# Performance work log

Measured on AMD Instinct MI355X. Metric: run time of the kernel, lower is better.

Reference implementation:

```python
import jax, jax.numpy as jnp
import numpy as np

N = 50000      # nodes (single node type 'tx')
E = 400000     # edges per edge type ('fwd' and 'rev')
F_IN = 128     # input feature dim
F = 128        # cfg.gnn.dim_inner
H = 8          # attention heads
D = F // H     # per-head dim
L = 2          # cfg.gnn.layers_mp
C = 2          # dim_out (fraud logits)


def setup_inputs() -> dict:
    key = jax.random.key(0)
    k = jax.random.split(key, 12)
    f32 = jnp.float32
    g = lambda kk, sh, fan: jax.random.normal(kk, sh, f32) / np.float32(np.sqrt(fan))
    return dict(
        x=jax.random.normal(k[0], (N, F_IN), f32),
        edge_index_fwd=jax.random.randint(k[1], (2, E), 0, N),
        edge_index_rev=jax.random.randint(k[2], (2, E), 0, N),
        in_w=g(k[3], (F_IN, F), F_IN),
        in_b=jnp.zeros((F,), f32),
        kqv_w=g(k[4], (L, F, 3 * F), F),
        kqv_b=jnp.zeros((L, 3 * F), f32),
        krel_w=g(k[5], (L, 2, H, D, D), D),
        vrel_w=g(k[6], (L, 2, H, D, D), D),
        p_rel=jnp.ones((L, 2, H), f32),
        out_w=g(k[7], (L, F, F), F),
        out_b=jnp.zeros((L, F), f32),
        skip=jnp.ones((L,), f32),
        head_w=g(k[8], (F, C), F),
        head_b=jnp.zeros((C,), f32),
    )


def reference(x, edge_index_fwd, edge_index_rev, in_w, in_b, kqv_w, kqv_b,
              krel_w, vrel_w, p_rel, out_w, out_b, skip, head_w, head_b):
    n = x.shape[0]
    ef, er = edge_index_fwd, edge_index_rev
    Ef, Er = ef.shape[1], er.shape[1]
    dst = jnp.concatenate([ef[1], er[1]])                 # [E_tot]
    scale = 1.0 / jnp.sqrt(jnp.asarray(D, x.dtype))

    h = x @ in_w + in_b                                   # in_proj['tx'], [N,F]
    for l in range(L):
        kqv = h @ kqv_w[l] + kqv_b[l]                     # [N,3F]
        k, q, v = jnp.split(kqv, 3, axis=1)
        k = k.reshape(n, H, D)
        q = q.reshape(n, H, D)
        v = v.reshape(n, H, D)
        # per-edge-type relation transforms (head-wise DxD, no bias)
        k_rel = jnp.einsum('nhd,ehdf->enhf', k, krel_w[l])  # [2,N,H,D]
        v_rel = jnp.einsum('nhd,ehdf->enhf', v, vrel_w[l])
        # gather src features per edge type, concatenate edge types
        k_j = jnp.concatenate([k_rel[0][ef[0]], k_rel[1][er[0]]], axis=0)  # [E_tot,H,D]
        v_j = jnp.concatenate([v_rel[0][ef[0]], v_rel[1][er[0]]], axis=0)
        p_e = jnp.concatenate([jnp.broadcast_to(p_rel[l, 0], (Ef, H)),
                               jnp.broadcast_to(p_rel[l, 1], (Er, H))], axis=0)
        q_i = q[dst]                                       # [E_tot,H,D]
        alpha = jnp.einsum('ehd,ehd->eh', q_i, k_j) * p_e * scale
        # segment softmax over all incoming edges of each dst node
        m = jax.ops.segment_max(alpha, dst, num_segments=n)
        ex = jnp.exp(alpha - m[dst])
        denom = jax.ops.segment_sum(ex, dst, num_segments=n)
        w = ex / (denom[dst] + 1e-16)                      # [E_tot,H]
        agg = jax.ops.segment_sum(w[:, :, None] * v_j, dst,
                                  num_segments=n).reshape(n, F)
        a = jax.nn.gelu(agg, approximate=False) @ out_w[l] + out_b[l]
        g = jax.nn.sigmoid(skip[l])
        h = jax.nn.relu(g * a + (1.0 - g) * h)             # skip + act(dropout=0)
    return h @ head_w + head_b                             # logits [N,C]
```

## Files before the change

### kernel.cpp

```cpp
#include <hip/hip_runtime.h>
#include <math.h>

typedef short short8 __attribute__((ext_vector_type(8)));
typedef float f32x4 __attribute__((ext_vector_type(4)));

__device__ __forceinline__ unsigned short f2bf(float f){
    unsigned u = __float_as_uint(f);
    unsigned r = u + 0x7fffu + ((u >> 16) & 1u);
    return (unsigned short)(r >> 16);
}

__global__ void k_zero_i(int* __restrict__ p, int n)
{
    for (int i = blockIdx.x*blockDim.x + threadIdx.x; i < n; i += gridDim.x*blockDim.x)
        p[i] = 0;
}

__global__ void k_count(const int* __restrict__ ef, const int* __restrict__ er,
                        int* __restrict__ deg, int Ef, int Er)
{
    int Etot = Ef + Er;
    for (int e = blockIdx.x*blockDim.x + threadIdx.x; e < Etot; e += gridDim.x*blockDim.x) {
        int dst = (e < Ef) ? ef[Ef + e] : er[Er + (e - Ef)];
        atomicAdd(&deg[dst], 1);
    }
}

__global__ void k_chunk_sums(const int* __restrict__ deg, int* __restrict__ csum, int n)
{
    __shared__ int s[256];
    int t = threadIdx.x, i = blockIdx.x*256 + t;
    s[t] = (i < n) ? deg[i] : 0;
    __syncthreads();
    for (int off = 128; off > 0; off >>= 1) {
        if (t < off) s[t] += s[t + off];
        __syncthreads();
    }
    if (t == 0) csum[blockIdx.x] = s[0];
}

__global__ void k_scan_chunks(int* __restrict__ csum, int nch)
{
    __shared__ int s[1024];
    int t = threadIdx.x;
    int v = (t < nch) ? csum[t] : 0;
    s[t] = v; __syncthreads();
    for (int off = 1; off < 1024; off <<= 1) {
        int u = (t >= off) ? s[t - off] : 0;
        __syncthreads();
        s[t] += u;
        __syncthreads();
    }
    if (t < nch) csum[t] = s[t] - v;
}

__global__ void k_rowstart(const int* __restrict__ deg, const int* __restrict__ csum,
                           int* __restrict__ row_start, int* __restrict__ cursor, int n)
{
    __shared__ int s[256];
    int t = threadIdx.x, i = blockIdx.x*256 + t;
    int d = (i < n) ? deg[i] : 0;
    s[t] = d; __syncthreads();
    for (int off = 1; off < 256; off <<= 1) {
        int u = (t >= off) ? s[t - off] : 0;
        __syncthreads();
        s[t] += u;
        __syncthreads();
    }
    if (i <= n) {
        int rs = csum[blockIdx.x] + s[t] - d;
        row_start[i] = rs;
        cursor[i] = rs;
    }
}

__global__ void k_fill(const int* __restrict__ ef, const int* __restrict__ er,
                       int* __restrict__ cursor, unsigned* __restrict__ srcs,
                       int Ef, int Er, int n_nodes)
{
    int Etot = Ef + Er;
    if (blockIdx.x == 0 && threadIdx.x == 0) { srcs[Etot] = 0; srcs[Etot + 1] = 0; }
    for (int e = blockIdx.x*blockDim.x + threadIdx.x; e < Etot; e += gridDim.x*blockDim.x) {
        int src, dst, tt;
        if (e < Ef) { src = ef[e]; dst = ef[Ef + e]; tt = 0; }
        else { int e2 = e - Ef; src = er[e2]; dst = er[Er + e2]; tt = 1; }
        int pos = atomicAdd(&cursor[dst], 1);
        srcs[pos] = (unsigned)(tt*n_nodes + src)*32u;
    }
}

__global__ void k_cast(const float* __restrict__ src, unsigned short* __restrict__ dst,
                       long long n)
{
    for (long long i = (long long)blockIdx.x*blockDim.x + threadIdx.x; i*4 < n;
         i += (long long)gridDim.x*blockDim.x) {
        float4 v = *(const float4*)&src[i*4];
        uint2 w;
        w.x = (unsigned)f2bf(v.x) | ((unsigned)f2bf(v.y) << 16);
        w.y = (unsigned)f2bf(v.z) | ((unsigned)f2bf(v.w) << 16);
        *(uint2*)&dst[i*4] = w;
    }
}

__global__ void k_wt(const float* __restrict__ Wf, unsigned short* __restrict__ WT, int C)
{
    int idx = blockIdx.x*blockDim.x + threadIdx.x;
    if (idx >= 128*C) return;
    int r = idx / C, c = idx % C;
    WT[(size_t)c*128 + r] = f2bf(Wf[(size_t)r*C + c]);
}

__global__ void k_compose(const float* __restrict__ kqv_w, const float* __restrict__ kqv_b,
                          const float* __restrict__ krel_w, const float* __restrict__ vrel_w,
                          const float* __restrict__ p_rel, unsigned short* __restrict__ WcT,
                          float* __restrict__ biasc)
{
    int idx = blockIdx.x*blockDim.x + threadIdx.x;
    int tot = 2*129*640;
    if (idx >= tot) return;
    int l = idx / (129*640);
    int rem = idx % (129*640);
    int r = rem / 640, c = rem % 640;
    float val;
    if (c < 128) {
        val = (r < 128) ? kqv_w[((size_t)l*128 + r)*384 + 128 + c]
                        : kqv_b[l*384 + 128 + c];
    } else {
        int c2 = c - 128;
        int tt = c2 >> 8;
        int cc = c2 & 255;
        int f = cc >> 1;
        int part = cc & 1;
        int hh = f >> 4, fd = f & 15;
        const float* rw = (part == 0 ? krel_w : vrel_w)
                          + (((size_t)(l*2 + tt)*8 + hh)*16)*16 + fd;
        int base_col = (part == 0 ? 0 : 256) + hh*16;
        float s = 0.f;
        #pragma unroll
        for (int d = 0; d < 16; ++d) {
            float a = (r < 128) ? kqv_w[((size_t)l*128 + r)*384 + base_col + d]
                                : kqv_b[l*384 + base_col + d];
            s += a * rw[d*16];
        }
        if (part == 0) s *= p_rel[(l*2 + tt)*8 + hh] * 0.25f * 1.4426950408889634f;
        val = s;
    }
    if (r < 128) WcT[((size_t)l*640 + c)*128 + r] = f2bf(val);
    else         biasc[l*640 + c] = val;
}

__global__ void k_compose_out(const float* __restrict__ out_w, const float* __restrict__ out_b,
                              unsigned short* __restrict__ WoT, float* __restrict__ biaso)
{
    int idx = blockIdx.x*blockDim.x + threadIdx.x;
    int tot = 2*129*128;
    if (idx >= tot) return;
    int l = idx / (129*128);
    int rem = idx % (129*128);
    int r = rem / 128, c = rem % 128;
    if (r < 128) WoT[((size_t)l*128 + c)*128 + r] = f2bf(out_w[((size_t)l*128 + r)*128 + c]);
    else         biaso[l*128 + c] = out_b[l*128 + c];
}

__global__ __launch_bounds__(256) void k_mfma(
    const unsigned short* __restrict__ A16, const unsigned short* __restrict__ WT,
    const float* __restrict__ biasc, float* __restrict__ out_f,
    unsigned short* __restrict__ out_b16, unsigned* __restrict__ kv,
    const float* __restrict__ skip, int l,
    int n_nodes, int R, int C, int mode)
{
    __shared__ uint4 As[64*16];
    __shared__ uint4 Ws[64*16];
    int b = blockIdx.x;
    int xcd = b & 7, jj = b >> 3;
    int r_t = (jj / C)*8 + xcd;
    int c_t = jj % C;
    if (r_t >= R) return;
    int n0 = r_t*64, c0 = c_t*64;
    int t = threadIdx.x;

    #pragma unroll
    for (int it = 0; it < 4; ++it) {
        int gi = t + it*256;
        int m = gi >> 4, g = gi & 15;
        uint4 a = *(const uint4*)&A16[((size_t)(n0 + m)*16 + g)*8];
        As[m*16 + (g ^ (m & 15))] = a;
    }
    #pragma unroll
    for (int it = 0; it < 4; ++it) {
        int gi = t + it*256;
        int cw = gi >> 4, g = gi & 15;
        uint4 wv = *(const uint4*)&WT[((size_t)(c0 + cw)*16 + g)*8];
        Ws[cw*16 + (g ^ (cw & 15))] = wv;
    }
    __syncthreads();

    int lane = t & 63, w = t >> 6;
    int lm = lane & 15, quad = lane >> 4;
    f32x4 acc[4];
    #pragma unroll
    for (int i = 0; i < 4; ++i) { acc[i][0]=0.f; acc[i][1]=0.f; acc[i][2]=0.f; acc[i][3]=0.f; }

    #pragma unroll
    for (int chunk = 0; chunk < 4; ++chunk) {
        int gq = chunk*4 + quad;
        short8 bfrag = *(const short8*)&Ws[(w*16 + lm)*16 + (gq ^ lm)];
        #pragma unroll
        for (int i = 0; i < 4; ++i) {
            short8 afrag = *(const short8*)&As[(i*16 + lm)*16 + (gq ^ lm)];
            acc[i] = __builtin_amdgcn_mfma_f32_16x16x32_bf16(afrag, bfrag, acc[i], 0, 0, 0);
        }
    }

    int c = c0 + w*16 + lm;
    float bc = biasc[c];
    if (mode == 2) {
        float g = 1.f/(1.f + expf(-skip[l]));
        #pragma unroll
        for (int i = 0; i < 4; ++i) {
            #pragma unroll
            for (int rr = 0; rr < 4; ++rr) {
                int m = n0 + i*16 + quad*4 + rr;
                if (m < n_nodes) {
                    size_t o = (size_t)m*128 + c;
                    float hv = out_f[o];
                    float nv = fmaxf(g*(acc[i][rr] + bc) + (1.f - g)*hv, 0.f);
                    out_f[o] = nv;
                    out_b16[o] = f2bf(nv);
                }
            }
        }
    } else if (mode == 0) {
        #pragma unroll
        for (int i = 0; i < 4; ++i) {
            #pragma unroll
            for (int rr = 0; rr < 4; ++rr) {
                int m = n0 + i*16 + quad*4 + rr;
                if (m < n_nodes) {
                    size_t o = (size_t)m*128 + c;
                    float nv = acc[i][rr] + bc;
                    out_f[o] = nv;
                    out_b16[o] = f2bf(nv);
                }
            }
        }
    } else if (c0 < 128) {
        #pragma unroll
        for (int i = 0; i < 4; ++i) {
            #pragma unroll
            for (int rr = 0; rr < 4; ++rr) {
                int m = n0 + i*16 + quad*4 + rr;
                if (m < n_nodes) out_f[(size_t)m*128 + c] = acc[i][rr] + bc;
            }
        }
    } else {
        int c2 = c - 128;
        int tt = c2 >> 8;
        int f = (c2 & 255) >> 1;
        unsigned* dst = kv + (size_t)tt*n_nodes*128;
        bool isk = (lane & 1) == 0;
        #pragma unroll
        for (int i = 0; i < 4; ++i) {
            #pragma unroll
            for (int rr = 0; rr < 4; ++rr) {
                float val = acc[i][rr] + bc;
                float other = __shfl_xor(val, 1);
                int m = n0 + i*16 + quad*4 + rr;
                if (isk && m < n_nodes) {
                    unsigned wd = ((unsigned)f2bf(val) << 16) | (unsigned)f2bf(other);
                    dst[(size_t)m*128 + f] = wd;
                }
            }
        }
    }
}

__global__ __launch_bounds__(256) void k_attn(
    const unsigned* __restrict__ srcs, const int* __restrict__ row_start,
    const uint4* __restrict__ kv, const float* __restrict__ qa,
    unsigned short* __restrict__ qa16, int n_nodes)
{
    int lane = threadIdx.x & 31;
    int n = blockIdx.x*8 + (threadIdx.x >> 5);
    if (n >= n_nodes) return;
    float4 q4 = *(const float4*)&qa[(size_t)n*128 + lane*4];
    int s = row_start[n], e = row_start[n + 1];

    float m0 = -INFINITY, l0 = 0.f; float4 a0 = make_float4(0.f,0.f,0.f,0.f);
    float m1 = -INFINITY, l1 = 0.f; float4 a1 = make_float4(0.f,0.f,0.f,0.f);

    uint4 w0n = kv[srcs[s] + lane];
    uint4 w1n = kv[srcs[s + 1] + lane];
    int pos = s;
    for (; pos + 1 < e; pos += 2) {
        uint4 w0 = w0n, w1 = w1n;
        unsigned sv0 = srcs[pos + 2], sv1 = srcs[pos + 3];
        w0n = kv[sv0 + lane];
        w1n = kv[sv1 + lane];
        float d0 = __uint_as_float(w0.x & 0xffff0000u)*q4.x
                 + __uint_as_float(w0.y & 0xffff0000u)*q4.y
                 + __uint_as_float(w0.z & 0xffff0000u)*q4.z
                 + __uint_as_float(w0.w & 0xffff0000u)*q4.w;
        float d1 = __uint_as_float(w1.x & 0xffff0000u)*q4.x
                 + __uint_as_float(w1.y & 0xffff0000u)*q4.y
                 + __uint_as_float(w1.z & 0xffff0000u)*q4.z
                 + __uint_as_float(w1.w & 0xffff0000u)*q4.w;
        d0 += __shfl_xor(d0, 1); d1 += __shfl_xor(d1, 1);
        d0 += __shfl_xor(d0, 2); d1 += __shfl_xor(d1, 2);
        float mn0 = fmaxf(m0, d0), mn1 = fmaxf(m1, d1);
        float sc0 = exp2f(m0 - mn0), sc1 = exp2f(m1 - mn1);
        float wt0 = exp2f(d0 - mn0), wt1 = exp2f(d1 - mn1);
        l0 = l0*sc0 + wt0;               l1 = l1*sc1 + wt1;
        a0.x = a0.x*sc0 + wt0*__uint_as_float(w0.x << 16);
        a1.x = a1.x*sc1 + wt1*__uint_as_float(w1.x << 16);
        a0.y = a0.y*sc0 + wt0*__uint_as_float(w0.y << 16);
        a1.y = a1.y*sc1 + wt1*__uint_as_float(w1.y << 16);
        a0.z = a0.z*sc0 + wt0*__uint_as_float(w0.z << 16);
        a1.z = a1.z*sc1 + wt1*__uint_as_float(w1.z << 16);
        a0.w = a0.w*sc0 + wt0*__uint_as_float(w0.w << 16);
        a1.w = a1.w*sc1 + wt1*__uint_as_float(w1.w << 16);
        m0 = mn0; m1 = mn1;
    }
    if (pos < e) {
        uint4 w0 = w0n;
        float d = __uint_as_float(w0.x & 0xffff0000u)*q4.x
                + __uint_as_float(w0.y & 0xffff0000u)*q4.y
                + __uint_as_float(w0.z & 0xffff0000u)*q4.z
                + __uint_as_float(w0.w & 0xffff0000u)*q4.w;
        d += __shfl_xor(d, 1);
        d += __shfl_xor(d, 2);
        float mn = fmaxf(m0, d);
        float sc = exp2f(m0 - mn);
        float wt = exp2f(d - mn);
        l0 = l0*sc + wt;
        a0.x = a0.x*sc + wt*__uint_as_float(w0.x << 16);
        a0.y = a0.y*sc + wt*__uint_as_float(w0.y << 16);
        a0.z = a0.z*sc + wt*__uint_as_float(w0.z << 16);
        a0.w = a0.w*sc + wt*__uint_as_float(w0.w << 16);
        m0 = mn;
    }
    float mn = fmaxf(m0, m1);
    float sc0 = (m0 == -INFINITY) ? 0.f : exp2f(m0 - mn);
    float sc1 = (m1 == -INFINITY) ? 0.f : exp2f(m1 - mn);
    float lsum = l0*sc0 + l1*sc1;
    float4 acc;
    acc.x = a0.x*sc0 + a1.x*sc1;
    acc.y = a0.y*sc0 + a1.y*sc1;
    acc.z = a0.z*sc0 + a1.z*sc1;
    acc.w = a0.w*sc0 + a1.w*sc1;

    float inv = 1.f/(lsum + 1e-16f);
    float x0 = acc.x*inv, x1 = acc.y*inv, x2 = acc.z*inv, x3 = acc.w*inv;
    float g0 = 0.5f*x0*(1.f + erff(x0*0.70710678118654752f));
    float g1 = 0.5f*x1*(1.f + erff(x1*0.70710678118654752f));
    float g2 = 0.5f*x2*(1.f + erff(x2*0.70710678118654752f));
    float g3 = 0.5f*x3*(1.f + erff(x3*0.70710678118654752f));
    uint2 pk;
    pk.x = (unsigned)f2bf(g0) | ((unsigned)f2bf(g1) << 16);
    pk.y = (unsigned)f2bf(g2) | ((unsigned)f2bf(g3) << 16);
    *(uint2*)&qa16[(size_t)n*128 + lane*4] = pk;
}

__global__ __launch_bounds__(256) void k_head(
    const float* __restrict__ h, const float* __restrict__ hw,
    const float* __restrict__ hb, float* __restrict__ out, int n_nodes)
{
    int n = blockIdx.x*4 + (threadIdx.x >> 6);
    if (n >= n_nodes) return;
    int t = threadIdx.x & 63;
    float h0 = h[(size_t)n*128 + t], h1 = h[(size_t)n*128 + 64 + t];
    float c0 = h0*hw[t*2]     + h1*hw[(t+64)*2];
    float c1 = h0*hw[t*2 + 1] + h1*hw[(t+64)*2 + 1];
    for (int off = 32; off > 0; off >>= 1) {
        c0 += __shfl_down(c0, off);
        c1 += __shfl_down(c1, off);
    }
    if (t == 0) {
        out[n*2]     = c0 + hb[0];
        out[n*2 + 1] = c1 + hb[1];
    }
}

extern "C" void kernel_launch(void* const* d_in, const int* in_sizes, int n_in,
                              void* d_out, int out_size, void* d_ws, size_t ws_size,
                              hipStream_t stream)
{
    const float* x      = (const float*)d_in[0];
    const int*   ef     = (const int*)d_in[1];
    const int*   er     = (const int*)d_in[2];
    const float* in_w   = (const float*)d_in[3];
    const float* in_b   = (const float*)d_in[4];
    const float* kqv_w  = (const float*)d_in[5];
    const float* kqv_b  = (const float*)d_in[6];
    const float* krel_w = (const float*)d_in[7];
    const float* vrel_w = (const float*)d_in[8];
    const float* p_rel  = (const float*)d_in[9];
    const float* out_w  = (const float*)d_in[10];
    const float* out_b  = (const float*)d_in[11];
    const float* skip   = (const float*)d_in[12];
    const float* head_w = (const float*)d_in[13];
    const float* head_b = (const float*)d_in[14];
    float* out = (float*)d_out;

    int n_nodes = in_sizes[0] / 128;
    int Ef = in_sizes[1] / 2, Er = in_sizes[2] / 2;
    int Etot = Ef + Er;
    int nch = (n_nodes + 255)/256;
    int ntile = (n_nodes + 63)/64;
    int npad = ntile*64;

    float* p = (float*)d_ws;
    float* h    = p; p += (size_t)npad*128;
    float* qa   = p; p += (size_t)npad*128;
    unsigned* kv = (unsigned*)p; p += (size_t)2*n_nodes*128;
    unsigned short* h16  = (unsigned short*)p; p += (size_t)npad*128/2;
    unsigned short* qa16 = (unsigned short*)p; p += (size_t)npad*128/2;
    unsigned short* x16  = (unsigned short*)p; p += (size_t)npad*128/2;
    unsigned short* WiT = (unsigned short*)p; p += (size_t)(128*128)/2;
    unsigned short* WcT = (unsigned short*)p; p += (size_t)(2*640*128)/2;
    float* biasc = p; p += 2*640;
    unsigned short* WoT = (unsigned short*)p; p += (size_t)(2*128*128)/2;
    float* biaso = p; p += 2*128;
    int* deg       = (int*)p;      p += n_nodes;
    int* csum      = (int*)p;      p += 1024;
    int* row_start = (int*)p;      p += n_nodes + 1;
    int* cursor    = (int*)p;      p += n_nodes + 1;
    unsigned* srcs = (unsigned*)p; p += Etot + 2;

    int Rg = (ntile + 7)/8;

    k_zero_i<<<(n_nodes + 255)/256, 256, 0, stream>>>(deg, n_nodes);
    k_count<<<1024, 256, 0, stream>>>(ef, er, deg, Ef, Er);
    k_chunk_sums<<<nch, 256, 0, stream>>>(deg, csum, n_nodes);
    k_scan_chunks<<<1, 1024, 0, stream>>>(csum, nch);
    k_rowstart<<<(n_nodes + 256)/256, 256, 0, stream>>>(deg, csum, row_start, cursor, n_nodes);
    k_fill<<<1024, 256, 0, stream>>>(ef, er, cursor, srcs, Ef, Er, n_nodes);
    k_compose<<<(2*129*640 + 255)/256, 256, 0, stream>>>(kqv_w, kqv_b, krel_w, vrel_w,
                                                         p_rel, WcT, biasc);
    k_compose_out<<<(2*129*128 + 255)/256, 256, 0, stream>>>(out_w, out_b, WoT, biaso);
    k_wt<<<(128*128 + 255)/256, 256, 0, stream>>>(in_w, WiT, 128);
    k_cast<<<2048, 256, 0, stream>>>(x, x16, (long long)n_nodes*128);

    k_mfma<<<Rg*8*2, 256, 0, stream>>>(x16, WiT, in_b, h, h16, kv, skip, 0,
                                       n_nodes, ntile, 2, 0);
    for (int l = 0; l < 2; ++l) {
        k_mfma<<<Rg*8*10, 256, 0, stream>>>(h16, WcT + (size_t)l*640*128,
                                            biasc + l*640, qa, nullptr, kv, skip, l,
                                            n_nodes, ntile, 10, 1);
        k_attn<<<(n_nodes + 7)/8, 256, 0, stream>>>(srcs, row_start,
                                                    (const uint4*)kv, qa, qa16, n_nodes);
        k_mfma<<<Rg*8*2, 256, 0, stream>>>(qa16, WoT + (size_t)l*128*128,
                                           biaso + l*128, h, h16, kv, skip, l,
                                           n_nodes, ntile, 2, 2);
    }
    k_head<<<(n_nodes + 3)/4, 256, 0, stream>>>(h, head_w, head_b, out, n_nodes);
}
```

Measured before the change: 442.7 us.

## Merge setup kernels into one launch and fuse head projection into final GEMM

Five small preprocessing kernels (weight composition, out-weight transpose, input-weight transpose, x cast to bf16, degree zeroing) are merged into a single grid-stride setup kernel, which also initialises the logits with the head bias. The separate head kernel is removed. The last output-projection GEMM now computes the two logits in its epilogue via shuffle reductions and atomicAdd, so the final h no longer has to be written and reread. This cuts kernel launches and one pass over h, at the cost of float atomics (nondeterministic summation order) and branchy setup code.

```diff
diff --git a/kernel.cpp b/kernel.cpp
--- a/kernel.cpp
+++ b/kernel.cpp
@@ -8,12 +8,6 @@
     unsigned u = __float_as_uint(f);
     unsigned r = u + 0x7fffu + ((u >> 16) & 1u);
     return (unsigned short)(r >> 16);
-}
-
-__global__ void k_zero_i(int* __restrict__ p, int n)
-{
-    for (int i = blockIdx.x*blockDim.x + threadIdx.x; i < n; i += gridDim.x*blockDim.x)
-        p[i] = 0;
 }
 
 __global__ void k_count(const int* __restrict__ ef, const int* __restrict__ er,
@@ -89,84 +83,89 @@
     }
 }
 
-__global__ void k_cast(const float* __restrict__ src, unsigned short* __restrict__ dst,
-                       long long n)
-{
-    for (long long i = (long long)blockIdx.x*blockDim.x + threadIdx.x; i*4 < n;
-         i += (long long)gridDim.x*blockDim.x) {
-        float4 v = *(const float4*)&src[i*4];
-        uint2 w;
-        w.x = (unsigned)f2bf(v.x) | ((unsigned)f2bf(v.y) << 16);
-        w.y = (unsigned)f2bf(v.z) | ((unsigned)f2bf(v.w) << 16);
-        *(uint2*)&dst[i*4] = w;
-    }
-}
-
-__global__ void k_wt(const float* __restrict__ Wf, unsigned short* __restrict__ WT, int C)
-{
-    int idx = blockIdx.x*blockDim.x + threadIdx.x;
-    if (idx >= 128*C) return;
-    int r = idx / C, c = idx % C;
-    WT[(size_t)c*128 + r] = f2bf(Wf[(size_t)r*C + c]);
-}
-
-__global__ void k_compose(const float* __restrict__ kqv_w, const float* __restrict__ kqv_b,
-                          const float* __restrict__ krel_w, const float* __restrict__ vrel_w,
-                          const float* __restrict__ p_rel, unsigned short* __restrict__ WcT,
-                          float* __restrict__ biasc)
-{
-    int idx = blockIdx.x*blockDim.x + threadIdx.x;
-    int tot = 2*129*640;
-    if (idx >= tot) return;
-    int l = idx / (129*640);
-    int rem = idx % (129*640);
-    int r = rem / 640, c = rem % 640;
-    float val;
-    if (c < 128) {
-        val = (r < 128) ? kqv_w[((size_t)l*128 + r)*384 + 128 + c]
-                        : kqv_b[l*384 + 128 + c];
-    } else {
-        int c2 = c - 128;
-        int tt = c2 >> 8;
-        int cc = c2 & 255;
-        int f = cc >> 1;
-        int part = cc & 1;
-        int hh = f >> 4, fd = f & 15;
-        const float* rw = (part == 0 ? krel_w : vrel_w)
-                          + (((size_t)(l*2 + tt)*8 + hh)*16)*16 + fd;
-        int base_col = (part == 0 ? 0 : 256) + hh*16;
-        float s = 0.f;
-        #pragma unroll
-        for (int d = 0; d < 16; ++d) {
-            float a = (r < 128) ? kqv_w[((size_t)l*128 + r)*384 + base_col + d]
-                                : kqv_b[l*384 + base_col + d];
-            s += a * rw[d*16];
-        }
-        if (part == 0) s *= p_rel[(l*2 + tt)*8 + hh] * 0.25f * 1.4426950408889634f;
-        val = s;
-    }
-    if (r < 128) WcT[((size_t)l*640 + c)*128 + r] = f2bf(val);
-    else         biasc[l*640 + c] = val;
-}
-
-__global__ void k_compose_out(const float* __restrict__ out_w, const float* __restrict__ out_b,
-                              unsigned short* __restrict__ WoT, float* __restrict__ biaso)
-{
-    int idx = blockIdx.x*blockDim.x + threadIdx.x;
-    int tot = 2*129*128;
-    if (idx >= tot) return;
-    int l = idx / (129*128);
-    int rem = idx % (129*128);
-    int r = rem / 128, c = rem % 128;
-    if (r < 128) WoT[((size_t)l*128 + c)*128 + r] = f2bf(out_w[((size_t)l*128 + r)*128 + c]);
-    else         biaso[l*128 + c] = out_b[l*128 + c];
+__global__ void k_setup(const float* __restrict__ kqv_w, const float* __restrict__ kqv_b,
+                        const float* __restrict__ krel_w, const float* __restrict__ vrel_w,
+                        const float* __restrict__ p_rel, const float* __restrict__ out_w,
+                        const float* __restrict__ out_b, const float* __restrict__ in_w,
+                        const float* __restrict__ x, const float* __restrict__ head_b,
+                        unsigned short* __restrict__ WcT, float* __restrict__ biasc,
+                        unsigned short* __restrict__ WoT, float* __restrict__ biaso,
+                        unsigned short* __restrict__ WiT, unsigned short* __restrict__ x16,
+                        int* __restrict__ deg, float* __restrict__ logits, int n_nodes)
+{
+    const int N0 = 2*129*640;
+    const int N1 = N0 + 2*129*128;
+    const int N2 = N1 + 128*128;
+    const long long N3 = (long long)N2 + (long long)n_nodes*32;
+    const long long N4 = N3 + n_nodes;
+    const long long N5 = N4 + 2*n_nodes;
+
+    for (long long idx = (long long)blockIdx.x*blockDim.x + threadIdx.x; idx < N5;
+         idx += (long long)gridDim.x*blockDim.x) {
+        if (idx < N0) {
+            int i = (int)idx;
+            int l = i / (129*640);
+            int rem = i % (129*640);
+            int r = rem / 640, c = rem % 640;
+            float val;
+            if (c < 128) {
+                val = (r < 128) ? kqv_w[((size_t)l*128 + r)*384 + 128 + c]
+                                : kqv_b[l*384 + 128 + c];
+            } else {
+                int c2 = c - 128;
+                int tt = c2 >> 8;
+                int cc = c2 & 255;
+                int f = cc >> 1;
+                int part = cc & 1;
+                int hh = f >> 4, fd = f & 15;
+                const float* rw = (part == 0 ? krel_w : vrel_w)
+                                  + (((size_t)(l*2 + tt)*8 + hh)*16)*16 + fd;
+                int base_col = (part == 0 ? 0 : 256) + hh*16;
+                float s = 0.f;
+                #pragma unroll
+                for (int d = 0; d < 16; ++d) {
+                    float a = (r < 128) ? kqv_w[((size_t)l*128 + r)*384 + base_col + d]
+                                        : kqv_b[l*384 + base_col + d];
+                    s += a * rw[d*16];
+                }
+                if (part == 0) s *= p_rel[(l*2 + tt)*8 + hh] * 0.25f * 1.4426950408889634f;
+                val = s;
+            }
+            if (r < 128) WcT[((size_t)l*640 + c)*128 + r] = f2bf(val);
+            else         biasc[l*640 + c] = val;
+        } else if (idx < N1) {
+            int i = (int)(idx - N0);
+            int l = i / (129*128);
+            int rem = i % (129*128);
+            int r = rem / 128, c = rem % 128;
+            if (r < 128) WoT[((size_t)l*128 + c)*128 + r] = f2bf(out_w[((size_t)l*128 + r)*128 + c]);
+            else         biaso[l*128 + c] = out_b[l*128 + c];
+        } else if (idx < N2) {
+            int i = (int)(idx - N1);
+            int r = i >> 7, c = i & 127;
+            WiT[(size_t)c*128 + r] = f2bf(in_w[(size_t)r*128 + c]);
+        } else if (idx < N3) {
+            long long i = idx - N2;
+            float4 v = *(const float4*)&x[i*4];
+            uint2 w;
+            w.x = (unsigned)f2bf(v.x) | ((unsigned)f2bf(v.y) << 16);
+            w.y = (unsigned)f2bf(v.z) | ((unsigned)f2bf(v.w) << 16);
+            *(uint2*)&x16[i*4] = w;
+        } else if (idx < N4) {
+            deg[idx - N3] = 0;
+        } else {
+            long long i = idx - N4;
+            logits[i] = head_b[i & 1];
+        }
+    }
 }
 
 __global__ __launch_bounds__(256) void k_mfma(
     const unsigned short* __restrict__ A16, const unsigned short* __restrict__ WT,
     const float* __restrict__ biasc, float* __restrict__ out_f,
     unsigned short* __restrict__ out_b16, unsigned* __restrict__ kv,
-    const float* __restrict__ skip, int l,
+    const float* __restrict__ skip, const float* __restrict__ hw,
+    float* __restrict__ logits, int l,
     int n_nodes, int R, int C, int mode)
 {
     __shared__ uint4 As[64*16];
@@ -214,7 +213,31 @@
 
     int c = c0 + w*16 + lm;
     float bc = biasc[c];
-    if (mode == 2) {
+    if (mode == 3) {
+        float g = 1.f/(1.f + expf(-skip[l]));
+        float hw0 = hw[c*2], hw1 = hw[c*2 + 1];
+        #pragma unroll
+        for (int i = 0; i < 4; ++i) {
+            #pragma unroll
+            for (int rr = 0; rr < 4; ++rr) {
+                int m = n0 + i*16 + quad*4 + rr;
+                float nv = 0.f;
+                if (m < n_nodes) {
+                    float hv = out_f[(size_t)m*128 + c];
+                    nv = fmaxf(g*(acc[i][rr] + bc) + (1.f - g)*hv, 0.f);
+                }
+                float p0 = nv*hw0, p1 = nv*hw1;
+                p0 += __shfl_xor(p0, 1); p1 += __shfl_xor(p1, 1);
+                p0 += __shfl_xor(p0, 2); p1 += __shfl_xor(p1, 2);
+                p0 += __shfl_xor(p0, 4); p1 += __shfl_xor(p1, 4);
+                p0 += __shfl_xor(p0, 8); p1 += __shfl_xor(p1, 8);
+                if (lm == 0 && m < n_nodes) {
+                    atomicAdd(&logits[m*2],     p0);
+                    atomicAdd(&logits[m*2 + 1], p1);
+                }
+            }
+        }
+    } else if (mode == 2) {
         float g = 1.f/(1.f + expf(-skip[l]));
         #pragma unroll
         for (int i = 0; i < 4; ++i) {
@@ -361,26 +384,6 @@
     *(uint2*)&qa16[(size_t)n*128 + lane*4] = pk;
 }
 
-__global__ __launch_bounds__(256) void k_head(
-    const float* __restrict__ h, const float* __restrict__ hw,
-    const float* __restrict__ hb, float* __restrict__ out, int n_nodes)
-{
-    int n = blockIdx.x*4 + (threadIdx.x >> 6);
-    if (n >= n_nodes) return;
-    int t = threadIdx.x & 63;
-    float h0 = h[(size_t)n*128 + t], h1 = h[(size_t)n*128 + 64 + t];
-    float c0 = h0*hw[t*2]     + h1*hw[(t+64)*2];
-    float c1 = h0*hw[t*2 + 1] + h1*hw[(t+64)*2 + 1];
-    for (int off = 32; off > 0; off >>= 1) {
-        c0 += __shfl_down(c0, off);
-        c1 += __shfl_down(c1, off);
-    }
-    if (t == 0) {
-        out[n*2]     = c0 + hb[0];
-        out[n*2 + 1] = c1 + hb[1];
-    }
-}
-
 extern "C" void kernel_launch(void* const* d_in, const int* in_sizes, int n_in,
                               void* d_out, int out_size, void* d_ws, size_t ws_size,
                               hipStream_t stream)
@@ -429,29 +432,26 @@
 
     int Rg = (ntile + 7)/8;
 
-    k_zero_i<<<(n_nodes + 255)/256, 256, 0, stream>>>(deg, n_nodes);
+    k_setup<<<7500, 256, 0, stream>>>(kqv_w, kqv_b, krel_w, vrel_w, p_rel, out_w, out_b,
+                                      in_w, x, head_b, WcT, biasc, WoT, biaso, WiT, x16,
+                                      deg, out, n_nodes);
     k_count<<<1024, 256, 0, stream>>>(ef, er, deg, Ef, Er);
     k_chunk_sums<<<nch, 256, 0, stream>>>(deg, csum, n_nodes);
     k_scan_chunks<<<1, 1024, 0, stream>>>(csum, nch);
     k_rowstart<<<(n_nodes + 256)/256, 256, 0, stream>>>(deg, csum, row_start, cursor, n_nodes);
     k_fill<<<1024, 256, 0, stream>>>(ef, er, cursor, srcs, Ef, Er, n_nodes);
-    k_compose<<<(2*129*640 + 255)/256, 256, 0, stream>>>(kqv_w, kqv_b, krel_w, vrel_w,
-                                                         p_rel, WcT, biasc);
-    k_compose_out<<<(2*129*128 + 255)/256, 256, 0, stream>>>(out_w, out_b, WoT, biaso);
-    k_wt<<<(128*128 + 255)/256, 256, 0, stream>>>(in_w, WiT, 128);
-    k_cast<<<2048, 256, 0, stream>>>(x, x16, (long long)n_nodes*128);
-
-    k_mfma<<<Rg*8*2, 256, 0, stream>>>(x16, WiT, in_b, h, h16, kv, skip, 0,
+
+    k_mfma<<<Rg*8*2, 256, 0, stream>>>(x16, WiT, in_b, h, h16, kv, skip, head_w, out, 0,
                                        n_nodes, ntile, 2, 0);
     for (int l = 0; l < 2; ++l) {
         k_mfma<<<Rg*8*10, 256, 0, stream>>>(h16, WcT + (size_t)l*640*128,
-                                            biasc + l*640, qa, nullptr, kv, skip, l,
-                                            n_nodes, ntile, 10, 1);
+                                            biasc + l*640, qa, nullptr, kv, skip,
+                                            head_w, out, l, n_nodes, ntile, 10, 1);
         k_attn<<<(n_nodes + 7)/8, 256, 0, stream>>>(srcs, row_start,
                                                     (const uint4*)kv, qa, qa16, n_nodes);
+        int omode = (l == 1) ? 3 : 2;
         k_mfma<<<Rg*8*2, 256, 0, stream>>>(qa16, WoT + (size_t)l*128*128,
-                                           biaso + l*128, h, h16, kv, skip, l,
-                                           n_nodes, ntile, 2, 2);
-    }
-    k_head<<<(n_nodes + 3)/4, 256, 0, stream>>>(h, head_w, head_b, out, n_nodes);
-}
+                                           biaso + l*128, h, h16, kv, skip,
+                                           head_w, out, l, n_nodes, ntile, 2, omode);
+    }
+}
```

Measured after the change: 444.9 us. No clear change (+0.5%).
